# Optimization experiments

Measured on AMD Instinct MI355X. Metric: run time of the kernel, lower is better.

Reference implementation:

```python
import jax, jax.numpy as jnp
import numpy as np

T, B, OBS, H, A = 512, 64, 512, 1024, 18


def setup_inputs() -> dict:
    key = jax.random.key(0)
    ks = jax.random.split(key, 8)
    s = lambda fan: 1.0 / np.sqrt(fan)
    return {
        "obs": jax.random.normal(ks[0], (T, B, OBS), jnp.float32),
        # binary done/valid mask per (timestep, env)
        "mask": (jax.random.uniform(ks[1], (T, B)) > 0.05).astype(jnp.float32),
        "W_enc": jax.random.normal(ks[2], (H, OBS), jnp.float32) * s(OBS),
        "b_enc": jnp.zeros((H,), jnp.float32),
        "W_ih": jax.random.normal(ks[3], (4 * H, H), jnp.float32) * s(H),
        "b_ih": jnp.zeros((4 * H,), jnp.float32),
        "W_hh": jax.random.normal(ks[4], (4 * H, H), jnp.float32) * s(H),
        "b_hh": jnp.zeros((4 * H,), jnp.float32),
        "W_dec": jax.random.normal(ks[5], (A, H), jnp.float32) * s(H),
        "b_dec": jnp.zeros((A,), jnp.float32),
    }


def reference(obs, mask, W_enc, b_enc, W_ih, b_ih, W_hh, b_hh, W_dec, b_dec):
    # encoder MLP + relu, batched over all T*B (one big GEMM)
    encoded = jax.nn.relu(jnp.einsum("tbo,ho->tbh", obs, W_enc) + b_enc)
    # precompute input contribution to LSTM gates for all timesteps: [T,B,4H]
    x_gates = jnp.einsum("tbh,gh->tbg", encoded, W_ih) + b_ih + b_hh

    def step(carry, inp):
        h, c = carry
        xg, m = inp  # xg: [B,4H], m: [B]
        gates = xg + h @ W_hh.T
        i, f, g, o = jnp.split(gates, 4, axis=-1)  # torch LSTMCell order
        c_new = jax.nn.sigmoid(f) * c + jax.nn.sigmoid(i) * jnp.tanh(g)
        h_new = jax.nn.sigmoid(o) * jnp.tanh(c_new)
        m = m[:, None]
        h_new = h_new * m
        c_new = c_new * m
        return (h_new, c_new), h_new

    h0 = jnp.zeros((B, H), jnp.float32)
    c0 = jnp.zeros((B, H), jnp.float32)
    (h, c), latent = jax.lax.scan(step, (h0, c0), (x_gates, mask))

    # decoder over flattened (T*B, H) then mask q-values
    values = jnp.einsum("tbh,ah->tba", latent, W_dec) + b_dec
    values = values * mask[..., None]
    return values, h, c
```

## Files before the change

### kernel.cpp

```cpp
#include <hip/hip_runtime.h>
#include <hip/hip_bf16.h>

#define T_ 512
#define B_ 64
#define OBS_ 512
#define H_ 1024
#define A_ 18
#define MM_ (T_*B_)
#define G4_ (4*H_)
#define CH_ 64
#define NCH_ (T_/CH_)
#define CM_ (CH_*B_)

typedef unsigned short u16;
typedef unsigned long long u64;
typedef __attribute__((ext_vector_type(8))) short s8v;
typedef __attribute__((ext_vector_type(4))) float f4v;

__device__ __forceinline__ float b2f(u16 u){
    unsigned x = ((unsigned)u) << 16;
    return __builtin_bit_cast(float, x);
}
__device__ __forceinline__ u16 f2b(float f){
    unsigned x = __builtin_bit_cast(unsigned, f);
    return (u16)((x + 0x7fffu + ((x >> 16) & 1u)) >> 16);
}

__device__ __forceinline__ float fsig(float x){
    return __builtin_amdgcn_rcpf(1.f + __expf(-x));
}
__device__ __forceinline__ float ftanh(float x){
    return 1.f - 2.f * __builtin_amdgcn_rcpf(__expf(2.f * x) + 1.f);
}


__global__ void prep_all(const float* __restrict__ Wenc, const float* __restrict__ Wih,
                         const float* __restrict__ Whh, const float* __restrict__ Wdec,
                         const float* __restrict__ bih, const float* __restrict__ bhh,
                         u16* __restrict__ wenc_b, u16* __restrict__ wih_b,
                         u16* __restrict__ whh_b, u16* __restrict__ wdec_b,
                         float* __restrict__ bias2, u16* __restrict__ h0buf,
                         float* __restrict__ c_f32, unsigned* __restrict__ flags)
{
    int i = blockIdx.x * blockDim.x + threadIdx.x;
    int stride = gridDim.x * blockDim.x;
    for (int k = i; k < G4_ * H_; k += stride){
        wih_b[k] = f2b(Wih[k]);
        whh_b[k] = f2b(Whh[k]);
    }
    for (int k = i; k < H_ * OBS_; k += stride) wenc_b[k] = f2b(Wenc[k]);
    for (int k = i; k < A_ * H_; k += stride) wdec_b[k] = f2b(Wdec[k]);
    for (int k = i; k < G4_; k += stride) bias2[k] = bih[k] + bhh[k];
    unsigned* h0 = (unsigned*)h0buf;
    for (int k = i; k < B_ * H_ / 2; k += stride) h0[k] = 0u;
    for (int k = i; k < B_ * H_; k += stride) c_f32[k] = 0.f;
    for (int k = i; k < 1024; k += stride) flags[k] = 0u;
}

__global__ void copy_hc(const float* __restrict__ h, const float* __restrict__ c,
                        float* __restrict__ out){
    int i = blockIdx.x * blockDim.x + threadIdx.x;
    out[(size_t)MM_*A_ + i] = h[i];
    out[(size_t)MM_*A_ + B_*H_ + i] = c[i];
}


#define LDSS 72

__global__ __launch_bounds__(256) void gemm_enc(
    const float* __restrict__ A, const u16* __restrict__ W,
    const float* __restrict__ bias, u16* __restrict__ C,
    int M, int N, int K)
{
    __shared__ __align__(16) u16 As[128 * LDSS];
    __shared__ __align__(16) u16 Bs[128 * LDSS];

    const int tid  = threadIdx.x;
    const int lane = tid & 63;
    const int wid  = tid >> 6;
    const int wm   = wid & 1, wn = wid >> 1;
    const int m0   = blockIdx.y * 128, n0 = blockIdx.x * 128;
    const int quad = lane >> 4, l16 = lane & 15;

    f4v acc[4][4];
    #pragma unroll
    for (int i = 0; i < 4; i++)
        #pragma unroll
        for (int j = 0; j < 4; j++) acc[i][j] = (f4v){0.f,0.f,0.f,0.f};

    for (int k0 = 0; k0 < K; k0 += 64){
        __syncthreads();
        #pragma unroll
        for (int pss = 0; pss < 8; pss++){
            int idx = pss * 256 + tid;
            int row = idx >> 4, ch = idx & 15;
            float4 v = *(const float4*)(A + (size_t)(m0 + row) * K + k0 + ch * 4);
            u16* d = &As[row * LDSS + ch * 4];
            d[0] = f2b(v.x); d[1] = f2b(v.y); d[2] = f2b(v.z); d[3] = f2b(v.w);
        }
        #pragma unroll
        for (int pss = 0; pss < 4; pss++){
            int idx = pss * 256 + tid;
            int row = idx >> 3, ch = idx & 7;
            *(uint4*)&Bs[row * LDSS + ch * 8] =
                *(const uint4*)(W + (size_t)(n0 + row) * K + k0 + ch * 8);
        }
        __syncthreads();

        #pragma unroll
        for (int kk = 0; kk < 64; kk += 32){
            s8v af[4], bf[4];
            #pragma unroll
            for (int mt = 0; mt < 4; mt++)
                af[mt] = *(const s8v*)&As[(wm*64 + mt*16 + l16) * LDSS + kk + quad*8];
            #pragma unroll
            for (int nt = 0; nt < 4; nt++)
                bf[nt] = *(const s8v*)&Bs[(wn*64 + nt*16 + l16) * LDSS + kk + quad*8];
            #pragma unroll
            for (int mt = 0; mt < 4; mt++)
                #pragma unroll
                for (int nt = 0; nt < 4; nt++)
                    acc[mt][nt] = __builtin_amdgcn_mfma_f32_16x16x32_bf16(
                        af[mt], bf[nt], acc[mt][nt], 0, 0, 0);
        }
    }

    #pragma unroll
    for (int mt = 0; mt < 4; mt++){
        #pragma unroll
        for (int nt = 0; nt < 4; nt++){
            #pragma unroll
            for (int r = 0; r < 4; r++){
                int m = m0 + wm*64 + mt*16 + quad*4 + r;
                int n = n0 + wn*64 + nt*16 + l16;
                C[(size_t)m * N + n] = f2b(fmaxf(acc[mt][nt][r] + bias[n], 0.f));
            }
        }
    }
}


__global__ __launch_bounds__(256, 1) void lstm_scan(
    const u16* __restrict__ enc,
    const u16* __restrict__ Wih,
    const u16* __restrict__ Whh,
    const float* __restrict__ bias2,
    u16* __restrict__ h_hist,
    float* __restrict__ c_glob,
    float* __restrict__ h_f32,
    const float* __restrict__ mask,
    unsigned* __restrict__ flags,
    int t0, int nsteps, u16* __restrict__ seed)
{
    __shared__ float red[4][4][16][24];

    const int tid  = threadIdx.x;
    const int lane = tid & 63;
    const int w    = tid >> 6;
    const int quad = lane >> 4, l16 = lane & 15;
    const int bid  = blockIdx.x;
    const int g = bid & 3, s = bid >> 2;
    const int rb0 = g * 16, j0 = s * 16;

    const int koff = w * 256;
    s8v bf[4][8], wf[4][8];
    #pragma unroll
    for (int gate = 0; gate < 4; gate++)
        #pragma unroll
        for (int ks = 0; ks < 8; ks++){
            size_t off = (size_t)(gate * H_ + j0 + l16) * H_ + koff + ks * 32 + quad * 8;
            bf[gate][ks] = *(const s8v*)(Whh + off);
            wf[gate][ks] = *(const s8v*)(Wih + off);
        }

    const int cb = tid >> 4, cu = tid & 15;
    const size_t cidx = (size_t)(rb0 + cb) * H_ + j0 + cu;
    float c_reg = c_glob[cidx];

    float br[4];
    #pragma unroll
    for (int gate = 0; gate < 4; gate++) br[gate] = bias2[gate * H_ + j0 + cu];

    const size_t hoff = (size_t)(rb0 + l16) * H_ + koff + quad * 8;
    const size_t eoff = hoff;

    unsigned* myflag = flags + (g << 8) + (s << 2) + w;
    const unsigned* pollp = flags + (g << 8) + (w << 6) + lane;

    s8v ef[8];
    f4v eacc[4];
    {
        const u16* es = enc + eoff;
        #pragma unroll
        for (int ks = 0; ks < 8; ks++) ef[ks] = *(const s8v*)(es + ks * 32);
        #pragma unroll
        for (int gate = 0; gate < 4; gate++) eacc[gate] = (f4v){0.f,0.f,0.f,0.f};
        #pragma unroll
        for (int ks = 0; ks < 8; ks++)
            #pragma unroll
            for (int gate = 0; gate < 4; gate++)
                eacc[gate] = __builtin_amdgcn_mfma_f32_16x16x32_bf16(
                    ef[ks], wf[gate][ks], eacc[gate], 0, 0, 0);
        if (nsteps > 1){
            const u16* en = enc + (size_t)B_ * H_ + eoff;
            #pragma unroll
            for (int ks = 0; ks < 8; ks++) ef[ks] = *(const s8v*)(en + ks * 32);
        }
    }
    float nm = mask[rb0 + cb];

    for (int st = 0; st < nsteps; st++){
        const float m = nm;

        #pragma unroll
        for (int gate = 0; gate < 4; gate++)
            #pragma unroll
            for (int ks = 0; ks < 8; ks++){
                asm volatile("" : "+v"(bf[gate][ks]));
                asm volatile("" : "+v"(wf[gate][ks]));
            }

        f4v acc[4];
        #pragma unroll
        for (int gate = 0; gate < 4; gate++) acc[gate] = eacc[gate];

        const unsigned tgt = (unsigned)(t0 + st);
        int tries = 0;
        for (;;){
            unsigned f = __hip_atomic_load(pollp, __ATOMIC_RELAXED, __HIP_MEMORY_SCOPE_AGENT);
            if (__all((int)(f >= tgt))) break;
            if (++tries > (1 << 20)) break;
            if (tries >= 8) __builtin_amdgcn_s_sleep(1);
        }

        const u16* hs = h_hist + (size_t)st * B_ * H_ + hoff;
        #pragma unroll
        for (int ks = 0; ks < 8; ks++){
            s8v af = *(const s8v*)(hs + ks * 32);
            #pragma unroll
            for (int gate = 0; gate < 4; gate++)
                acc[gate] = __builtin_amdgcn_mfma_f32_16x16x32_bf16(af, bf[gate][ks], acc[gate], 0, 0, 0);
        }
        #pragma unroll
        for (int gate = 0; gate < 4; gate++)
            #pragma unroll
            for (int r = 0; r < 4; r++)
                red[w][gate][quad * 4 + r][l16] = acc[gate][r];
        __syncthreads();

        float gi = br[0], gf = br[1], gg = br[2], go = br[3];
        #pragma unroll
        for (int ww = 0; ww < 4; ww++){
            gi += red[ww][0][cb][cu];
            gf += red[ww][1][cb][cu];
            gg += red[ww][2][cb][cu];
            go += red[ww][3][cb][cu];
        }

        float is = fsig(gi);
        float fs = fsig(gf);
        float os = fsig(go);
        float gt = ftanh(gg);

        float cn = fs * c_reg + is * gt;
        float hn = os * ftanh(cn);
        hn *= m; cn *= m;
        c_reg = cn;
        if (t0 + st == T_ - 1) h_f32[cidx] = hn;

        unsigned hb = (unsigned)f2b(hn);
        unsigned partner = (unsigned)__shfl_xor((int)hb, 1, 64);
        if ((cu & 1) == 0){
            unsigned packed = hb | (partner << 16);
            unsigned* dst = (unsigned*)(h_hist + (size_t)(st + 1) * B_ * H_ + cidx);
            __hip_atomic_store(dst, packed, __ATOMIC_RELAXED, __HIP_MEMORY_SCOPE_AGENT);
            if (seed && st == nsteps - 1){
                unsigned* dst0 = (unsigned*)(seed + cidx);
                __hip_atomic_store(dst0, packed, __ATOMIC_RELAXED, __HIP_MEMORY_SCOPE_AGENT);
            }
        }
        asm volatile("s_waitcnt vmcnt(0)" ::: "memory");

        if (lane == 0)
            __hip_atomic_store(myflag, (unsigned)(t0 + st + 1),
                               __ATOMIC_RELAXED, __HIP_MEMORY_SCOPE_AGENT);

        if (st + 1 < nsteps){
            #pragma unroll
            for (int gate = 0; gate < 4; gate++) eacc[gate] = (f4v){0.f,0.f,0.f,0.f};
            #pragma unroll
            for (int ks = 0; ks < 8; ks++)
                #pragma unroll
                for (int gate = 0; gate < 4; gate++)
                    eacc[gate] = __builtin_amdgcn_mfma_f32_16x16x32_bf16(
                        ef[ks], wf[gate][ks], eacc[gate], 0, 0, 0);
            if (st + 2 < nsteps){
                const u16* en = enc + (size_t)(st + 2) * B_ * H_ + eoff;
                #pragma unroll
                for (int ks = 0; ks < 8; ks++) ef[ks] = *(const s8v*)(en + ks * 32);
            }
            nm = mask[(size_t)(st + 1) * B_ + rb0 + cb];
        }

        __syncthreads();
    }

    c_glob[cidx] = c_reg;
}


__global__ __launch_bounds__(256) void decode_kernel(
    const u16* __restrict__ latent, const u16* __restrict__ Wdec,
    const float* __restrict__ bdec, const float* __restrict__ mask,
    float* __restrict__ values, int rows)
{
    __shared__ __align__(16) u16 wl[A_ * H_];
    const int tid = threadIdx.x;
    for (int i = tid; i < A_ * H_ / 8; i += 256)
        ((uint4*)wl)[i] = ((const uint4*)Wdec)[i];
    __syncthreads();

    const int lane = tid & 63;
    int wid = blockIdx.x * 4 + (tid >> 6);
    const int nwaves = gridDim.x * 4;

    for (int row = wid; row < rows; row += nwaves){
        float lat[16];
        #pragma unroll
        for (int i = 0; i < 16; i++)
            lat[i] = b2f(latent[(size_t)row * H_ + i*64 + lane]);
        float acc[A_];
        #pragma unroll
        for (int a = 0; a < A_; a++) acc[a] = 0.f;
        #pragma unroll
        for (int i = 0; i < 16; i++){
            #pragma unroll
            for (int a = 0; a < A_; a++)
                acc[a] += lat[i] * b2f(wl[a * H_ + i*64 + lane]);
        }
        float m = mask[row];
        #pragma unroll
        for (int a = 0; a < A_; a++){
            float v = acc[a];
            #pragma unroll
            for (int s = 32; s > 0; s >>= 1) v += __shfl_down(v, s, 64);
            if (lane == 0) values[(size_t)row * A_ + a] = (v + bdec[a]) * m;
        }
    }
}


extern "C" void kernel_launch(void* const* d_in, const int* in_sizes, int n_in,
                              void* d_out, int out_size, void* d_ws, size_t ws_size,
                              hipStream_t stream)
{
    const float* obs  = (const float*)d_in[0];
    const float* mask = (const float*)d_in[1];
    const float* Wenc = (const float*)d_in[2];
    const float* benc = (const float*)d_in[3];
    const float* Wih  = (const float*)d_in[4];
    const float* bih  = (const float*)d_in[5];
    const float* Whh  = (const float*)d_in[6];
    const float* bhh  = (const float*)d_in[7];
    const float* Wdec = (const float*)d_in[8];
    const float* bdec = (const float*)d_in[9];
    float* out = (float*)d_out;

    char* p = (char*)d_ws;
    size_t o = 0;
    auto alloc = [&](size_t bytes){ void* r = p + o; o += (bytes + 255) & ~(size_t)255; return r; };
    u16*      wenc_b  = (u16*)     alloc((size_t)H_ * OBS_ * 2);
    u16*      wih_b   = (u16*)     alloc((size_t)G4_ * H_ * 2);
    u16*      whh_b   = (u16*)     alloc((size_t)G4_ * H_ * 2);
    u16*      wdec_b  = (u16*)     alloc((size_t)A_ * H_ * 2);
    float*    bias2   = (float*)   alloc((size_t)G4_ * 4);
    float*    h_f32   = (float*)   alloc((size_t)B_ * H_ * 4);
    float*    c_f32   = (float*)   alloc((size_t)B_ * H_ * 4);
    unsigned* flags   = (unsigned*)alloc(1024 * 4);

    const size_t hall_b    = (size_t)(T_ + 1) * B_ * H_ * 2;
    const size_t enc_all_b = (size_t)MM_ * H_ * 2;
    const bool big = ws_size >= o + hall_b + enc_all_b + 65536;
    (void)in_sizes; (void)n_in; (void)out_size;

    if (big){
        u16* h_all   = (u16*)alloc(hall_b);
        u16* enc_all = (u16*)alloc(enc_all_b);

        prep_all<<<2048, 256, 0, stream>>>(Wenc, Wih, Whh, Wdec, bih, bhh,
                                           wenc_b, wih_b, whh_b, wdec_b,
                                           bias2, h_all, c_f32, flags);

        dim3 ge(H_ / 128, MM_ / 128);
        gemm_enc<<<ge, 256, 0, stream>>>(obs, wenc_b, benc, enc_all, MM_, H_, OBS_);

        lstm_scan<<<256, 256, 0, stream>>>(
            enc_all, wih_b, whh_b, bias2, h_all, c_f32, h_f32,
            mask, flags, 0, T_, nullptr);

        decode_kernel<<<4096, 256, 0, stream>>>(
            h_all + (size_t)B_ * H_, wdec_b, bdec, mask, out, MM_);
    } else {
        u16* h_hist = (u16*)alloc((size_t)(CH_ + 1) * B_ * H_ * 2);
        u16* enc_ch = (u16*)alloc((size_t)CM_ * H_ * 2);

        prep_all<<<2048, 256, 0, stream>>>(Wenc, Wih, Whh, Wdec, bih, bhh,
                                           wenc_b, wih_b, whh_b, wdec_b,
                                           bias2, h_hist, c_f32, flags);

        for (int c = 0; c < NCH_; c++){
            const int t0 = c * CH_;

            dim3 g1(H_ / 128, CM_ / 128);
            gemm_enc<<<g1, 256, 0, stream>>>(
                obs + (size_t)t0 * B_ * OBS_, wenc_b, benc, enc_ch, CM_, H_, OBS_);

            lstm_scan<<<256, 256, 0, stream>>>(
                enc_ch, wih_b, whh_b, bias2, h_hist, c_f32, h_f32,
                mask + (size_t)t0 * B_, flags, t0, CH_, h_hist);

            decode_kernel<<<256, 256, 0, stream>>>(
                h_hist + (size_t)B_ * H_, wdec_b, bdec, mask + (size_t)t0 * B_,
                out + (size_t)t0 * B_ * A_, CM_);
        }
    }

    copy_hc<<<256, 256, 0, stream>>>(h_f32, c_f32, out);
}
```

Baseline: 2.571 ms.

## Replace flag-based step sync with sentinel-valued h buffer polling

Drops the per-wave progress flags in the persistent LSTM scan. Every h history slot is instead pre-filled with an 0xFFFF bf16 sentinel, and consumers spin on the h data itself until no sentinel remains. This removes the vmcnt(0) wait and the flag store on the producer side, plus the separate flag load on the consumer side, shortening the per-step critical path. In exchange it must fill the whole h history with sentinels up front (and per chunk in the fallback path), and it relies on 0xFFFF (a NaN bf16) never being a real h value and on the per-dword atomic loads seeing complete 32-bit words. The LDS reduction padding also changes.

```diff
diff --git a/kernel.cpp b/kernel.cpp
--- a/kernel.cpp
+++ b/kernel.cpp
@@ -16,6 +16,7 @@
 typedef unsigned long long u64;
 typedef __attribute__((ext_vector_type(8))) short s8v;
 typedef __attribute__((ext_vector_type(4))) float f4v;
+typedef __attribute__((ext_vector_type(4))) unsigned u4v;
 
 __device__ __forceinline__ float b2f(u16 u){
     unsigned x = ((unsigned)u) << 16;
@@ -39,8 +40,8 @@
                          const float* __restrict__ bih, const float* __restrict__ bhh,
                          u16* __restrict__ wenc_b, u16* __restrict__ wih_b,
                          u16* __restrict__ whh_b, u16* __restrict__ wdec_b,
-                         float* __restrict__ bias2, u16* __restrict__ h0buf,
-                         float* __restrict__ c_f32, unsigned* __restrict__ flags)
+                         float* __restrict__ bias2, unsigned* __restrict__ hbuf,
+                         int zero_u32, int sent_u32, float* __restrict__ c_f32)
 {
     int i = blockIdx.x * blockDim.x + threadIdx.x;
     int stride = gridDim.x * blockDim.x;
@@ -51,10 +52,15 @@
     for (int k = i; k < H_ * OBS_; k += stride) wenc_b[k] = f2b(Wenc[k]);
     for (int k = i; k < A_ * H_; k += stride) wdec_b[k] = f2b(Wdec[k]);
     for (int k = i; k < G4_; k += stride) bias2[k] = bih[k] + bhh[k];
-    unsigned* h0 = (unsigned*)h0buf;
-    for (int k = i; k < B_ * H_ / 2; k += stride) h0[k] = 0u;
+    for (int k = i; k < zero_u32; k += stride) hbuf[k] = 0u;
+    for (int k = i; k < sent_u32; k += stride) hbuf[zero_u32 + k] = 0xFFFFFFFFu;
     for (int k = i; k < B_ * H_; k += stride) c_f32[k] = 0.f;
-    for (int k = i; k < 1024; k += stride) flags[k] = 0u;
+}
+
+__global__ void fill_sent(unsigned* __restrict__ p, int n){
+    int i = blockIdx.x * blockDim.x + threadIdx.x;
+    int stride = gridDim.x * blockDim.x;
+    for (int k = i; k < n; k += stride) p[k] = 0xFFFFFFFFu;
 }
 
 __global__ void copy_hc(const float* __restrict__ h, const float* __restrict__ c,
@@ -149,10 +155,9 @@
     float* __restrict__ c_glob,
     float* __restrict__ h_f32,
     const float* __restrict__ mask,
-    unsigned* __restrict__ flags,
     int t0, int nsteps, u16* __restrict__ seed)
 {
-    __shared__ float red[4][4][16][24];
+    __shared__ float red[4][4][16][17];
 
     const int tid  = threadIdx.x;
     const int lane = tid & 63;
@@ -184,9 +189,6 @@
     const size_t hoff = (size_t)(rb0 + l16) * H_ + koff + quad * 8;
     const size_t eoff = hoff;
 
-    unsigned* myflag = flags + (g << 8) + (s << 2) + w;
-    const unsigned* pollp = flags + (g << 8) + (w << 6) + lane;
-
     s8v ef[8];
     f4v eacc[4];
     {
@@ -212,35 +214,50 @@
     for (int st = 0; st < nsteps; st++){
         const float m = nm;
 
-        #pragma unroll
-        for (int gate = 0; gate < 4; gate++)
-            #pragma unroll
-            for (int ks = 0; ks < 8; ks++){
-                asm volatile("" : "+v"(bf[gate][ks]));
-                asm volatile("" : "+v"(wf[gate][ks]));
+        f4v acc[4];
+        #pragma unroll
+        for (int gate = 0; gate < 4; gate++) acc[gate] = eacc[gate];
+
+        const u16* hs = h_hist + (size_t)st * B_ * H_ + hoff;
+        s8v af[8];
+        #pragma unroll
+        for (int ks = 0; ks < 8; ks++) af[ks] = *(const s8v*)(hs + ks * 32);
+        {
+            int tries = 0;
+            for (;;){
+                bool bad = false;
+                #pragma unroll
+                for (int ks = 0; ks < 8; ks++){
+                    u4v uu = __builtin_bit_cast(u4v, af[ks]);
+                    #pragma unroll
+                    for (int j = 0; j < 4; j++){
+                        unsigned u = uu[j];
+                        bad |= ((u >> 16) == 0xFFFFu);
+                        bad |= ((u & 0xFFFFu) == 0xFFFFu);
+                    }
+                }
+                if (__all(!bad)) break;
+                if (++tries > (1 << 20)) break;
+                if (tries >= 4) __builtin_amdgcn_s_sleep(1);
+                #pragma unroll
+                for (int ks = 0; ks < 8; ks++){
+                    const unsigned* q = (const unsigned*)(hs + ks * 32);
+                    u4v uu;
+                    #pragma unroll
+                    for (int j = 0; j < 4; j++)
+                        uu[j] = __hip_atomic_load(q + j, __ATOMIC_RELAXED,
+                                                  __HIP_MEMORY_SCOPE_AGENT);
+                    af[ks] = __builtin_bit_cast(s8v, uu);
+                }
             }
-
-        f4v acc[4];
-        #pragma unroll
-        for (int gate = 0; gate < 4; gate++) acc[gate] = eacc[gate];
-
-        const unsigned tgt = (unsigned)(t0 + st);
-        int tries = 0;
-        for (;;){
-            unsigned f = __hip_atomic_load(pollp, __ATOMIC_RELAXED, __HIP_MEMORY_SCOPE_AGENT);
-            if (__all((int)(f >= tgt))) break;
-            if (++tries > (1 << 20)) break;
-            if (tries >= 8) __builtin_amdgcn_s_sleep(1);
-        }
-
-        const u16* hs = h_hist + (size_t)st * B_ * H_ + hoff;
-        #pragma unroll
-        for (int ks = 0; ks < 8; ks++){
-            s8v af = *(const s8v*)(hs + ks * 32);
+        }
+
+        #pragma unroll
+        for (int ks = 0; ks < 8; ks++)
             #pragma unroll
             for (int gate = 0; gate < 4; gate++)
-                acc[gate] = __builtin_amdgcn_mfma_f32_16x16x32_bf16(af, bf[gate][ks], acc[gate], 0, 0, 0);
-        }
+                acc[gate] = __builtin_amdgcn_mfma_f32_16x16x32_bf16(
+                    af[ks], bf[gate][ks], acc[gate], 0, 0, 0);
         #pragma unroll
         for (int gate = 0; gate < 4; gate++)
             #pragma unroll
@@ -279,11 +296,6 @@
                 __hip_atomic_store(dst0, packed, __ATOMIC_RELAXED, __HIP_MEMORY_SCOPE_AGENT);
             }
         }
-        asm volatile("s_waitcnt vmcnt(0)" ::: "memory");
-
-        if (lane == 0)
-            __hip_atomic_store(myflag, (unsigned)(t0 + st + 1),
-                               __ATOMIC_RELAXED, __HIP_MEMORY_SCOPE_AGENT);
 
         if (st + 1 < nsteps){
             #pragma unroll
@@ -376,7 +388,6 @@
     float*    bias2   = (float*)   alloc((size_t)G4_ * 4);
     float*    h_f32   = (float*)   alloc((size_t)B_ * H_ * 4);
     float*    c_f32   = (float*)   alloc((size_t)B_ * H_ * 4);
-    unsigned* flags   = (unsigned*)alloc(1024 * 4);
 
     const size_t hall_b    = (size_t)(T_ + 1) * B_ * H_ * 2;
     const size_t enc_all_b = (size_t)MM_ * H_ * 2;
@@ -388,15 +399,18 @@
         u16* enc_all = (u16*)alloc(enc_all_b);
 
         prep_all<<<2048, 256, 0, stream>>>(Wenc, Wih, Whh, Wdec, bih, bhh,
-                                           wenc_b, wih_b, whh_b, wdec_b,
-                                           bias2, h_all, c_f32, flags);
+                                           wenc_b, wih_b, whh_b, wdec_b, bias2,
+                                           (unsigned*)h_all,
+                                           B_ * H_ / 2,
+                                           T_ * B_ * H_ / 2,
+                                           c_f32);
 
         dim3 ge(H_ / 128, MM_ / 128);
         gemm_enc<<<ge, 256, 0, stream>>>(obs, wenc_b, benc, enc_all, MM_, H_, OBS_);
 
         lstm_scan<<<256, 256, 0, stream>>>(
             enc_all, wih_b, whh_b, bias2, h_all, c_f32, h_f32,
-            mask, flags, 0, T_, nullptr);
+            mask, 0, T_, nullptr);
 
         decode_kernel<<<4096, 256, 0, stream>>>(
             h_all + (size_t)B_ * H_, wdec_b, bdec, mask, out, MM_);
@@ -405,8 +419,9 @@
         u16* enc_ch = (u16*)alloc((size_t)CM_ * H_ * 2);
 
         prep_all<<<2048, 256, 0, stream>>>(Wenc, Wih, Whh, Wdec, bih, bhh,
-                                           wenc_b, wih_b, whh_b, wdec_b,
-                                           bias2, h_hist, c_f32, flags);
+                                           wenc_b, wih_b, whh_b, wdec_b, bias2,
+                                           (unsigned*)h_hist,
+                                           B_ * H_ / 2, CH_ * B_ * H_ / 2, c_f32);
 
         for (int c = 0; c < NCH_; c++){
             const int t0 = c * CH_;
@@ -415,9 +430,13 @@
             gemm_enc<<<g1, 256, 0, stream>>>(
                 obs + (size_t)t0 * B_ * OBS_, wenc_b, benc, enc_ch, CM_, H_, OBS_);
 
+            if (c > 0)
+                fill_sent<<<2048, 256, 0, stream>>>(
+                    (unsigned*)h_hist + B_ * H_ / 2, CH_ * B_ * H_ / 2);
+
             lstm_scan<<<256, 256, 0, stream>>>(
                 enc_ch, wih_b, whh_b, bias2, h_hist, c_f32, h_f32,
-                mask + (size_t)t0 * B_, flags, t0, CH_, h_hist);
+                mask + (size_t)t0 * B_, t0, CH_, h_hist);
 
             decode_kernel<<<256, 256, 0, stream>>>(
                 h_hist + (size_t)B_ * H_, wdec_b, bdec, mask + (size_t)t0 * B_,
```

After: 3.586 ms. 39.5% more time.
